# Performance work log

Hardware: AMD Instinct MI355X
Metric: run time of the kernel (lower is better)

The kernel has to match this reference:

```python
import jax, jax.numpy as jnp
import numpy as np

B, T, M, A, H, O = 32, 168, 1024, 8, 64, 1  # batch, time, map_units, num_attrs, hidden, outputs


def setup_inputs() -> dict:
    key = jax.random.key(0)
    ks = jax.random.split(key, 9)
    s = 0.05
    p = lambda k, shape: jax.random.normal(k, shape, dtype=jnp.float32) * s
    return {
        "input": jax.random.normal(ks[0], (B, T, M, A), dtype=jnp.float32),
        "assoc_w": p(ks[1], (M, A, H)),      # ICFA: per-map-unit attrs->hidden
        "assoc_b": p(ks[2], (M, H)),
        "w_ih": p(ks[3], (M, H, 4 * H)),     # per-map-unit LSTM cell weights
        "w_hh": p(ks[4], (M, H, 4 * H)),
        "b_ih": p(ks[5], (M, 4 * H)),
        "b_hh": p(ks[6], (M, 4 * H)),
        "dense_w": p(ks[7], (M, H, O)),      # per-map-unit output dense
        "dense_b": p(ks[8], (M, O)),
    }


def reference(input, assoc_w, assoc_b, w_ih, w_hh, b_ih, b_hh, dense_w, dense_b):
    x = jnp.transpose(input, (1, 0, 2, 3))  # [T,B,M,A] (batch_first -> time-major)
    b, m, h = x.shape[1], x.shape[2], assoc_w.shape[-1]
    h0 = jnp.zeros((b, m, h), x.dtype)
    c0 = jnp.zeros_like(h0)

    def step(carry, xt):
        hp, cp = carry
        # MaxMinNorm over attrs (keepdims so inverse broadcasts over hidden dim)
        mn = xt.min(-1, keepdims=True)
        mx = xt.max(-1, keepdims=True)
        yn = (xt - mn) / (mx - mn)                              # [B,M,A]
        # ICFA association layer: per-map-unit linear attrs -> hidden
        y = jnp.einsum("bma,mah->bmh", yn, assoc_w) + assoc_b   # [B,M,H]
        # per-map-unit LSTM cell (state carried, not fed to output per source)
        gates = (jnp.einsum("bmh,mhf->bmf", y, w_ih)
                 + jnp.einsum("bmh,mhf->bmf", hp, w_hh)
                 + b_ih + b_hh)                                  # [B,M,4H]
        i, f, g, o = jnp.split(gates, 4, axis=-1)
        cn = jax.nn.sigmoid(f) * cp + jax.nn.sigmoid(i) * jnp.tanh(g)
        hn = jax.nn.sigmoid(o) * jnp.tanh(cn)
        # inverse MaxMinNorm on assoc output
        y_inv = y * (mx - mn) + mn                               # [B,M,H]
        out = jnp.einsum("bmh,mho->bmo", y_inv, dense_w) + dense_b  # [B,M,O]
        return (hn, cn), out

    _, outs = jax.lax.scan(step, (h0, c0), x)   # [T,B,M,O]
    out = jnp.transpose(outs, (1, 0, 2, 3))     # [B,T,M,O]
    return out.squeeze(-1)
```

## Files before the change

### kernel.cpp

```cpp
#include <hip/hip_runtime.h>

#define B_ 32
#define T_ 168
#define M_ 1024
#define A_ 8
#define H_ 64


__global__ __launch_bounds__(256) void precompute_kernel(
    const float* __restrict__ assoc_w,
    const float* __restrict__ assoc_b,
    const float* __restrict__ dense_w,
    const float* __restrict__ dense_b,
    float* __restrict__ table)
{
    const int wave = threadIdx.x >> 6;
    const int lane = threadIdx.x & 63;
    const int m    = blockIdx.x * 4 + wave;
    if (m >= M_) return;

    const float dw = dense_w[m * H_ + lane];
    const float ab = assoc_b[m * H_ + lane];

    float v[A_];
#pragma unroll
    for (int a = 0; a < A_; ++a)
        v[a] = assoc_w[(m * A_ + a) * H_ + lane] * dw;
    float sb = ab * dw;
    float sd = dw;

#pragma unroll
    for (int off = 32; off >= 1; off >>= 1) {
#pragma unroll
        for (int a = 0; a < A_; ++a) v[a] += __shfl_xor(v[a], off, 64);
        sb += __shfl_xor(sb, off, 64);
        sd += __shfl_xor(sd, off, 64);
    }

    if (lane == 0) {
        float sv = 0.f;
#pragma unroll
        for (int a = 0; a < A_; ++a) { table[a * M_ + m] = v[a]; sv += v[a]; }
        table[8 * M_ + m]  = sd - sv - sb;
        table[9 * M_ + m]  = sb;
        table[10 * M_ + m] = dense_b[m];
    }
}

__global__ __launch_bounds__(256) void main_kernel(
    const float* __restrict__ x,
    const float* __restrict__ table,
    float* __restrict__ out,
    int n)
{
    const int idx = blockIdx.x * 256 + threadIdx.x;
    if (idx >= n) return;
    const int m = idx & (M_ - 1);

    const float4* xp = (const float4*)(x + (size_t)idx * A_);
    const float4 x0 = xp[0];
    const float4 x1 = xp[1];

    const float mn = fminf(fminf(fminf(x0.x, x0.y), fminf(x0.z, x0.w)),
                           fminf(fminf(x1.x, x1.y), fminf(x1.z, x1.w)));
    const float mx = fmaxf(fmaxf(fmaxf(x0.x, x0.y), fmaxf(x0.z, x0.w)),
                           fmaxf(fmaxf(x1.x, x1.y), fmaxf(x1.z, x1.w)));

    float dot;
    dot  = x0.x * table[0 * M_ + m];
    dot += x0.y * table[1 * M_ + m];
    dot += x0.z * table[2 * M_ + m];
    dot += x0.w * table[3 * M_ + m];
    dot += x1.x * table[4 * M_ + m];
    dot += x1.y * table[5 * M_ + m];
    dot += x1.z * table[6 * M_ + m];
    dot += x1.w * table[7 * M_ + m];

    out[idx] = dot + mn * table[8 * M_ + m] + mx * table[9 * M_ + m]
                   + table[10 * M_ + m];
}

__global__ __launch_bounds__(256) void fused_fallback_kernel(
    const float* __restrict__ x,
    const float* __restrict__ assoc_w,
    const float* __restrict__ assoc_b,
    const float* __restrict__ dense_w,
    const float* __restrict__ dense_b,
    float* __restrict__ out,
    int n)
{
    const int idx = blockIdx.x * 256 + threadIdx.x;
    if (idx >= n) return;
    const int m = idx & (M_ - 1);

    float v[A_] = {0.f};
    float sb = 0.f, sd = 0.f;
    for (int h = 0; h < H_; ++h) {
        const float dw = dense_w[m * H_ + h];
        sd += dw;
        sb += assoc_b[m * H_ + h] * dw;
#pragma unroll
        for (int a = 0; a < A_; ++a)
            v[a] += assoc_w[(m * A_ + a) * H_ + h] * dw;
    }
    float sv = 0.f;
#pragma unroll
    for (int a = 0; a < A_; ++a) sv += v[a];

    const float4* xp = (const float4*)(x + (size_t)idx * A_);
    const float4 x0 = xp[0];
    const float4 x1 = xp[1];
    const float xs[A_] = {x0.x, x0.y, x0.z, x0.w, x1.x, x1.y, x1.z, x1.w};

    float mn = xs[0], mx = xs[0], dot = 0.f;
#pragma unroll
    for (int a = 0; a < A_; ++a) {
        mn = fminf(mn, xs[a]);
        mx = fmaxf(mx, xs[a]);
        dot += xs[a] * v[a];
    }
    out[idx] = dot + mn * (sd - sv - sb) + mx * sb + dense_b[m];
}

extern "C" void kernel_launch(void* const* d_in, const int* in_sizes, int n_in,
                              void* d_out, int out_size, void* d_ws, size_t ws_size,
                              hipStream_t stream)
{
    const float* input   = (const float*)d_in[0];
    const float* assoc_w = (const float*)d_in[1];
    const float* assoc_b = (const float*)d_in[2];
    const float* dense_w = (const float*)d_in[7];
    const float* dense_b = (const float*)d_in[8];
    float* out = (float*)d_out;

    const int n = out_size;
    const size_t need = (size_t)(11 * M_) * sizeof(float);

    if (ws_size >= need) {
        float* table = (float*)d_ws;
        precompute_kernel<<<M_ / 4, 256, 0, stream>>>(assoc_w, assoc_b,
                                                      dense_w, dense_b, table);
        main_kernel<<<(n + 255) / 256, 256, 0, stream>>>(input, table, out, n);
    } else {
        fused_fallback_kernel<<<(n + 255) / 256, 256, 0, stream>>>(
            input, assoc_w, assoc_b, dense_w, dense_b, out, n);
    }
}
```

Before: 308.1 us.

## Process eight timesteps per thread and pack per-unit table into float4 rows

The coefficient table moves from an 11×M column layout to a 12-float per-map-unit row, so each thread loads its coefficients with three float4 reads. Each thread now handles eight (b,t) rows for one map unit, reusing those coefficients across all eight and issuing eight independent pairs of input loads for more memory-level parallelism. The kernel is bandwidth-bound on about 176 MB of input, so the gain likely comes from fewer table loads and better latency hiding. The cost is an eighth as many threads and higher register pressure.

```diff
diff --git a/kernel.cpp b/kernel.cpp
--- a/kernel.cpp
+++ b/kernel.cpp
@@ -5,6 +5,8 @@
 #define M_ 1024
 #define A_ 8
 #define H_ 64
+#define BT_ (B_ * T_)
+#define JT_ 8
 
 
 __global__ __launch_bounds__(256) void precompute_kernel(
@@ -39,45 +41,60 @@
 
     if (lane == 0) {
         float sv = 0.f;
+        float* t = table + m * 12;
 #pragma unroll
-        for (int a = 0; a < A_; ++a) { table[a * M_ + m] = v[a]; sv += v[a]; }
-        table[8 * M_ + m]  = sd - sv - sb;
-        table[9 * M_ + m]  = sb;
-        table[10 * M_ + m] = dense_b[m];
+        for (int a = 0; a < A_; ++a) { t[a] = v[a]; sv += v[a]; }
+        t[8]  = sd - sv - sb;
+        t[9]  = sb;
+        t[10] = dense_b[m];
+        t[11] = 0.f;
     }
 }
 
 __global__ __launch_bounds__(256) void main_kernel(
     const float* __restrict__ x,
     const float* __restrict__ table,
-    float* __restrict__ out,
-    int n)
+    float* __restrict__ out)
 {
-    const int idx = blockIdx.x * 256 + threadIdx.x;
-    if (idx >= n) return;
-    const int m = idx & (M_ - 1);
+    const int u = blockIdx.x * 256 + threadIdx.x;
+    const int m  = u & (M_ - 1);
+    const int g  = u >> 10;
+    if (g >= BT_ / JT_) return;
+    const int bt0 = g * JT_;
 
-    const float4* xp = (const float4*)(x + (size_t)idx * A_);
-    const float4 x0 = xp[0];
-    const float4 x1 = xp[1];
+    const float4* tp = (const float4*)(table + m * 12);
+    const float4 t0 = tp[0];
+    const float4 t1 = tp[1];
+    const float4 t2 = tp[2];
 
-    const float mn = fminf(fminf(fminf(x0.x, x0.y), fminf(x0.z, x0.w)),
-                           fminf(fminf(x1.x, x1.y), fminf(x1.z, x1.w)));
-    const float mx = fmaxf(fmaxf(fmaxf(x0.x, x0.y), fmaxf(x0.z, x0.w)),
-                           fmaxf(fmaxf(x1.x, x1.y), fmaxf(x1.z, x1.w)));
+    float4 xa[JT_], xb[JT_];
+#pragma unroll
+    for (int j = 0; j < JT_; ++j) {
+        const float4* xp =
+            (const float4*)(x + ((size_t)(bt0 + j) * M_ + m) * A_);
+        xa[j] = xp[0];
+        xb[j] = xp[1];
+    }
 
-    float dot;
-    dot  = x0.x * table[0 * M_ + m];
-    dot += x0.y * table[1 * M_ + m];
-    dot += x0.z * table[2 * M_ + m];
-    dot += x0.w * table[3 * M_ + m];
-    dot += x1.x * table[4 * M_ + m];
-    dot += x1.y * table[5 * M_ + m];
-    dot += x1.z * table[6 * M_ + m];
-    dot += x1.w * table[7 * M_ + m];
-
-    out[idx] = dot + mn * table[8 * M_ + m] + mx * table[9 * M_ + m]
-                   + table[10 * M_ + m];
+#pragma unroll
+    for (int j = 0; j < JT_; ++j) {
+        const float4 x0 = xa[j];
+        const float4 x1 = xb[j];
+        const float mn = fminf(fminf(fminf(x0.x, x0.y), fminf(x0.z, x0.w)),
+                               fminf(fminf(x1.x, x1.y), fminf(x1.z, x1.w)));
+        const float mx = fmaxf(fmaxf(fmaxf(x0.x, x0.y), fmaxf(x0.z, x0.w)),
+                               fmaxf(fmaxf(x1.x, x1.y), fmaxf(x1.z, x1.w)));
+        float dot;
+        dot  = x0.x * t0.x;
+        dot += x0.y * t0.y;
+        dot += x0.z * t0.z;
+        dot += x0.w * t0.w;
+        dot += x1.x * t1.x;
+        dot += x1.y * t1.y;
+        dot += x1.z * t1.z;
+        dot += x1.w * t1.w;
+        out[(size_t)(bt0 + j) * M_ + m] = dot + mn * t2.x + mx * t2.y + t2.z;
+    }
 }
 
 __global__ __launch_bounds__(256) void fused_fallback_kernel(
@@ -134,13 +151,14 @@
     float* out = (float*)d_out;
 
     const int n = out_size;
-    const size_t need = (size_t)(11 * M_) * sizeof(float);
+    const size_t need = (size_t)M_ * 12 * sizeof(float);
 
     if (ws_size >= need) {
         float* table = (float*)d_ws;
         precompute_kernel<<<M_ / 4, 256, 0, stream>>>(assoc_w, assoc_b,
                                                       dense_w, dense_b, table);
-        main_kernel<<<(n + 255) / 256, 256, 0, stream>>>(input, table, out, n);
+        const int total = M_ * (BT_ / JT_);
+        main_kernel<<<(total + 255) / 256, 256, 0, stream>>>(input, table, out);
     } else {
         fused_fallback_kernel<<<(n + 255) / 256, 256, 0, stream>>>(
             input, assoc_w, assoc_b, dense_w, dense_b, out, n);
```

Measured after the change: 317.6 us. 1.03x slower.
